# Kernel optimization log

Hardware: AMD Instinct MI355X
Metric: run time of the kernel (lower is better)

The kernel has to match this reference:

```python
import jax, jax.numpy as jnp
import numpy as np

DIM = 1024
Q_HEADS = 16
KV_HEADS = 4
DIM_HEAD = DIM // Q_HEADS  # 64
SOFTCLAMP = 50.0
EPS = 1e-8


def rotate_half(x):
    x_even = x[..., ::2]
    x_odd = x[..., 1::2]
    return jnp.stack([-x_odd, x_even], axis=-1).reshape(x.shape)


def setup_inputs() -> dict:
    key = jax.random.key(0)
    ks = jax.random.split(key, 10)
    B, S = 1, 2048
    dim_q = DIM_HEAD * Q_HEADS   # 1024
    dim_kv = DIM_HEAD * KV_HEADS  # 256
    std = 0.02
    x = jax.random.normal(ks[0], (B, S, DIM), dtype=jnp.float32)
    positions = jnp.broadcast_to(jnp.arange(S, dtype=jnp.int32)[None, :], (B, S))
    # causal mask: True = disallowed (torch semantics: allowed = ~attn_mask)
    attn_mask = jnp.triu(jnp.ones((S, S), dtype=bool), k=1)
    return {
        "x": x,
        "positions": positions,
        "attn_mask": attn_mask,
        "Wq": jax.random.normal(ks[1], (DIM, dim_q), jnp.float32) * std,
        "Wk": jax.random.normal(ks[2], (DIM, dim_kv), jnp.float32) * std,
        "Wv": jax.random.normal(ks[3], (DIM, dim_kv), jnp.float32) * std,
        "Wo": jax.random.normal(ks[4], (dim_q, DIM), jnp.float32) * std,
        "Wg": jax.random.normal(ks[5], (DIM, Q_HEADS), jnp.float32) * std,
        "Wm": jax.random.normal(ks[6], (DIM, KV_HEADS), jnp.float32) * std,
        "bm": jnp.zeros((KV_HEADS,), jnp.float32),
        "Wvr": jax.random.normal(ks[7], (DIM, dim_kv), jnp.float32) * std,
        "k_scale": jnp.ones((KV_HEADS, DIM_HEAD), jnp.float32),
    }


def reference(x, positions, attn_mask, Wq, Wk, Wv, Wo, Wg, Wm, bm, Wvr, k_scale):
    b, s, _ = x.shape
    h, qh, dh = KV_HEADS, Q_HEADS, DIM_HEAD
    g = qh // h

    q = (x @ Wq).reshape(b, s, qh, dh).transpose(0, 2, 1, 3)  # [b,qh,s,dh]
    k = (x @ Wk).reshape(b, s, h, dh).transpose(0, 2, 1, 3)   # [b,h,s,dh]
    v = (x @ Wv).reshape(b, s, h, dh).transpose(0, 2, 1, 3)

    # value-residual gating: v = lerp(v, residual_v, mix)
    residual_v = (x @ Wvr).reshape(b, s, h, dh).transpose(0, 2, 1, 3)
    mix = jax.nn.sigmoid(x @ Wm + bm).transpose(0, 2, 1)[..., None]  # [b,h,s,1]
    v = v + mix * (residual_v - v)

    # multi-head RMSNorm on k
    rms = jnp.sqrt(jnp.mean(k * k, axis=-1, keepdims=True) + EPS)
    k = k / rms * k_scale[None, :, None, :]

    # rotary embeddings (identical for all heads -> broadcast over head dim)
    inv_freq = 1.0 / (10000.0 ** (jnp.arange(0, dh, 2, dtype=jnp.float32) / dh))
    freqs = positions.astype(jnp.float32)[..., None] * inv_freq  # [b,s,dh/2]
    cos = jnp.repeat(jnp.cos(freqs), 2, axis=-1)[:, None, :, :]  # [b,1,s,dh]
    sin = jnp.repeat(jnp.sin(freqs), 2, axis=-1)[:, None, :, :]
    q = q * cos + rotate_half(q) * sin
    k = k * cos + rotate_half(k) * sin

    # grouped-query attention with softclamped scores
    scale = dh ** -0.5
    qg = q.reshape(b, h, g, s, dh)
    sim = jnp.einsum('bhgqd,bhkd->bhgqk', qg, k) * scale
    sim = jnp.tanh(sim / SOFTCLAMP) * SOFTCLAMP
    allowed = ~attn_mask  # [s,s]
    sim = jnp.where(allowed[None, None, None, :, :], sim, jnp.finfo(sim.dtype).min)
    attn = jax.nn.softmax(sim, axis=-1)
    out = jnp.einsum('bhgqk,bhkd->bhgqd', attn, v).reshape(b, qh, s, dh)

    # per-query-head sigmoid gates
    gates = jax.nn.sigmoid(x @ Wg).transpose(0, 2, 1)[..., None]  # [b,qh,s,1]
    out = out * gates

    out = out.transpose(0, 2, 1, 3).reshape(b, s, qh * dh)
    return out @ Wo
```

## Files before the change

kernel.cpp:

```cpp
#include <hip/hip_runtime.h>
#include <hip/hip_bf16.h>
#include <math.h>

typedef unsigned short u16;
typedef unsigned int u32;
typedef __attribute__((ext_vector_type(8))) __bf16 bf16x8;
typedef __attribute__((ext_vector_type(4))) float f32x4;

__device__ inline u16 f2bf(float f) {
  u32 b = __float_as_uint(f);
  b += 0x7FFFu + ((b >> 16) & 1u);
  return (u16)(b >> 16);
}
__device__ inline float bf2f(u16 b) { return __uint_as_float((u32)b << 16); }

__device__ __forceinline__ void gll16(const void* gp, void* lp) {
  __builtin_amdgcn_global_load_lds(
      (const __attribute__((address_space(1))) void*)gp,
      (__attribute__((address_space(3))) void*)lp, 16, 0, 0);
}

__global__ __launch_bounds__(256) void prep_all_k(
    const float* __restrict__ x, const int* __restrict__ positions,
    const float* __restrict__ Wq, const float* __restrict__ Wk,
    const float* __restrict__ Wv, const float* __restrict__ Wvr,
    const float* __restrict__ Wo, const float* __restrict__ Wg,
    const float* __restrict__ Wm, u16* __restrict__ xb,
    u16* __restrict__ WallT, u16* __restrict__ WoT, float* __restrict__ rtab) {
  __shared__ float tile[32][33];
  int bid = blockIdx.x, tid = threadIdx.x;
  if (bid < 1024) {
    int i = (bid * 256 + tid) * 8;
    float4 v0 = *(const float4*)&x[i];
    float4 v1 = *(const float4*)&x[i + 4];
    uint4 pk;
    pk.x = (u32)f2bf(v0.x) | ((u32)f2bf(v0.y) << 16);
    pk.y = (u32)f2bf(v0.z) | ((u32)f2bf(v0.w) << 16);
    pk.z = (u32)f2bf(v1.x) | ((u32)f2bf(v1.y) << 16);
    pk.w = (u32)f2bf(v1.z) | ((u32)f2bf(v1.w) << 16);
    *(uint4*)&xb[i] = pk;
    return;
  }
  if (bid >= 3968) {
    int idx = (bid - 3968) * 256 + tid;
    int s = idx >> 5, f = idx & 31;
    float inv = __expf(-(float)f * (9.210340371976184f / 32.f));
    float ang = (float)positions[s] * inv;
    rtab[(size_t)s * 64 + f] = cosf(ang);
    rtab[(size_t)s * 64 + 32 + f] = sinf(ang);
    return;
  }
  int b2 = bid - 1024;
  int k0 = (b2 & 31) * 32;
  int ybl = b2 >> 5;
  int tx = tid & 31, ty = tid >> 5;
  const float* src;
  int scol, sN, drow;
  u16* dst;
  if (ybl >= 60) {
    src = Wo; scol = (ybl - 60) * 32; sN = 1024; dst = WoT; drow = scol;
  } else {
    int n0 = ybl * 32;
    if (n0 >= 1792) {
#pragma unroll
      for (int j = 0; j < 4; ++j) {
        int n = n0 + ty * 4 + j, j2 = n - 1792, k = k0 + tx;
        float val = (j2 < 16) ? Wg[(size_t)k * 16 + j2]
                  : (j2 < 20) ? Wm[(size_t)k * 4 + (j2 - 16)] : 0.f;
        WallT[(size_t)n * 1024 + k] = f2bf(val);
      }
      return;
    }
    dst = WallT; drow = n0;
    if (n0 < 1024) { src = Wq; scol = n0; sN = 1024; }
    else if (n0 < 1280) { src = Wk; scol = n0 - 1024; sN = 256; }
    else if (n0 < 1536) { src = Wv; scol = n0 - 1280; sN = 256; }
    else { src = Wvr; scol = n0 - 1536; sN = 256; }
  }
#pragma unroll
  for (int j = 0; j < 4; ++j)
    tile[ty * 4 + j][tx] = src[(size_t)(k0 + ty * 4 + j) * sN + scol + tx];
  __syncthreads();
#pragma unroll
  for (int j = 0; j < 4; ++j)
    dst[(size_t)(drow + ty * 4 + j) * 1024 + k0 + tx] = f2bf(tile[tx][ty * 4 + j]);
}

template <int BM, bool BF16_OUT>
__global__ __launch_bounds__(512) void gemm_bf16_k(
    const u16* __restrict__ A, const u16* __restrict__ Bt, void* __restrict__ Cv,
    int M, int N, int K) {
  constexpr int MI = BM / 32;
  __shared__ __align__(16) u16 As[BM * 64];
  __shared__ __align__(16) u16 Bs[128 * 64];
  int tid = threadIdx.x;
  int w = tid >> 6, l = tid & 63;
  int wr = w >> 2, wc = w & 3;
  int lr = l & 15, lg = l >> 4;
  int lrow = l >> 3, lcol = (l & 7) * 8;
  int m0 = blockIdx.y * BM, n0 = blockIdx.x * 128;
  f32x4 zero = {0.f, 0.f, 0.f, 0.f};
  f32x4 acc[MI][2];
#pragma unroll
  for (int mi = 0; mi < MI; ++mi)
#pragma unroll
    for (int ni = 0; ni < 2; ++ni) acc[mi][ni] = zero;

  for (int kt = 0; kt < K; kt += 64) {
    __syncthreads();
#pragma unroll
    for (int t = 0; t < BM / 64; ++t) {
      int seg = t * 8 + w;
      gll16(&A[(size_t)(m0 + seg * 8 + lrow) * K + kt + lcol], &As[seg * 512]);
    }
#pragma unroll
    for (int t = 0; t < 2; ++t) {
      int seg = t * 8 + w;
      gll16(&Bt[(size_t)(n0 + seg * 8 + lrow) * K + kt + lcol], &Bs[seg * 512]);
    }
    __syncthreads();
#pragma unroll
    for (int kw = 0; kw < 2; ++kw) {
      bf16x8 af[MI], bfr[2];
#pragma unroll
      for (int mi = 0; mi < MI; ++mi)
        af[mi] = *(const bf16x8*)&As[(wr * (BM / 2) + mi * 16 + lr) * 64 + kw * 32 + lg * 8];
#pragma unroll
      for (int ni = 0; ni < 2; ++ni)
        bfr[ni] = *(const bf16x8*)&Bs[(wc * 32 + ni * 16 + lr) * 64 + kw * 32 + lg * 8];
#pragma unroll
      for (int mi = 0; mi < MI; ++mi)
#pragma unroll
        for (int ni = 0; ni < 2; ++ni)
          acc[mi][ni] = __builtin_amdgcn_mfma_f32_16x16x32_bf16(
              af[mi], bfr[ni], acc[mi][ni], 0, 0, 0);
    }
  }
#pragma unroll
  for (int mi = 0; mi < MI; ++mi)
#pragma unroll
    for (int ni = 0; ni < 2; ++ni)
#pragma unroll
      for (int r = 0; r < 4; ++r) {
        int row = m0 + wr * (BM / 2) + mi * 16 + lg * 4 + r;
        int col = n0 + wc * 32 + ni * 16 + lr;
        if (BF16_OUT)
          ((u16*)Cv)[(size_t)row * N + col] = f2bf(acc[mi][ni][r]);
        else
          ((float*)Cv)[(size_t)row * N + col] = acc[mi][ni][r];
      }
}

__global__ __launch_bounds__(256) void postproc_k(
    const float* __restrict__ bm, const float* __restrict__ ksc,
    const float* __restrict__ rtab, u16* __restrict__ qkvrb,
    u16* __restrict__ kb, u16* __restrict__ vb, float* __restrict__ g_out) {
  int s = blockIdx.x, tid = threadIdx.x;
  int lane = tid & 63, w = tid >> 6;
  u16* row = qkvrb + (size_t)s * 1920;
  const float* tr = rtab + (size_t)s * 64;
  if (tid < 16)
    g_out[s * 16 + tid] = 1.f / (1.f + __expf(-bf2f(row[1792 + tid])));
  int h = w, d = lane;
  float c = tr[d >> 1], sn = tr[32 + (d >> 1)];
  {
    float mixv = 1.f / (1.f + __expf(-(bf2f(row[1808 + h]) + bm[h])));
    float vv = bf2f(row[1280 + h * 64 + d]);
    float rv = bf2f(row[1536 + h * 64 + d]);
    vb[((size_t)h * 2048 + s) * 64 + d] = f2bf(vv + mixv * (rv - vv));
  }
  {
    float kv = bf2f(row[1024 + h * 64 + d]);
    float ss = kv * kv;
#pragma unroll
    for (int off = 32; off > 0; off >>= 1) ss += __shfl_xor(ss, off);
    float rms = sqrtf(ss * (1.f / 64.f) + 1e-8f);
    float kn = kv / rms * ksc[h * 64 + d];
    float partner = __shfl_xor(kn, 1);
    kb[((size_t)h * 2048 + s) * 64 + d] =
        f2bf((d & 1) ? fmaf(kn, c, partner * sn) : fmaf(kn, c, -partner * sn));
  }
#pragma unroll
  for (int r = 0; r < 4; ++r) {
    int e = r * 256 + tid;
    int dq = e & 63;
    float cq = tr[dq >> 1], sq = tr[32 + (dq >> 1)];
    float qv = bf2f(row[e]);
    float partner = __shfl_xor(qv, 1);
    float qr = (e & 1) ? fmaf(qv, cq, partner * sq) : fmaf(qv, cq, -partner * sq);
    row[e] = f2bf(qr * 0.125f);
  }
}

#define TPAD 66
__global__ __launch_bounds__(256) void vtrans_k(const u16* __restrict__ vb,
                                               u16* __restrict__ vtb) {
  __shared__ u16 tile[64 * TPAD];
  int h = blockIdx.y, s0 = blockIdx.x * 64;
  int t = threadIdx.x;
  {
    int r = t >> 2, cb = (t & 3) * 16;
    const u16* src = vb + ((size_t)h * 2048 + s0 + r) * 64 + cb;
    *(uint4*)&tile[r * TPAD + cb] = *(const uint4*)src;
    *(uint4*)&tile[r * TPAD + cb + 8] = *(const uint4*)(src + 8);
  }
  __syncthreads();
  int d = t >> 2, sb = (t & 3) * 16;
  u16 vals[16];
#pragma unroll
  for (int j = 0; j < 16; ++j) vals[j] = tile[(sb + j) * TPAD + d];
  uint4 a, b;
  a.x = (u32)vals[0] | ((u32)vals[1] << 16);
  a.y = (u32)vals[2] | ((u32)vals[3] << 16);
  a.z = (u32)vals[4] | ((u32)vals[5] << 16);
  a.w = (u32)vals[6] | ((u32)vals[7] << 16);
  b.x = (u32)vals[8] | ((u32)vals[9] << 16);
  b.y = (u32)vals[10] | ((u32)vals[11] << 16);
  b.z = (u32)vals[12] | ((u32)vals[13] << 16);
  b.w = (u32)vals[14] | ((u32)vals[15] << 16);
  u16* dst = vtb + ((size_t)h * 64 + d) * 2048 + s0 + sb;
  *(uint4*)dst = a;
  *(uint4*)(dst + 8) = b;
}

__global__ __launch_bounds__(512) void attn_k(
    const u16* __restrict__ qkvrb, const u16* __restrict__ kb,
    const u16* __restrict__ vtb, const float* __restrict__ g,
    u16* __restrict__ aob) {
  __shared__ __align__(16) u16 smem[40960];
  int head = blockIdx.x, hkv = head >> 2;
  int tid = threadIdx.x;
  int w = tid >> 6, l = tid & 63;
  int grp = w >> 2, wi = w & 3;
  int lr = l & 15, lg = l >> 4;
  int gtid = wi * 64 + l;
  u16* KsBase = smem + grp * 16384;
  u32* pw = (u32*)(smem + 32768) + (size_t)w * 512;
  float* mbuf = (float*)smem;
  f32x4 zero = {0.f, 0.f, 0.f, 0.f};
  const float C1 = 0.057707801635558534f;
  const float C2 = -144.26950408889634f;
  int sw = (lr & 7) << 2;
  int u0 = ((lg ^ (lr & 7)) << 3);
  int srow = l >> 3;
  int sunit = (l & 7) ^ srow;
  const u16* ksrc = kb + ((size_t)hkv * 2048 + srow) * 64 + sunit * 8;
  const u16* vsrc = vtb + ((size_t)(hkv * 64 + srow)) * 2048 + sunit * 8;
#pragma unroll 1
  for (int half = 0; half < 2; ++half) {
    int rb = half ? (int)blockIdx.y : (31 - (int)blockIdx.y);
    int row0 = rb * 64;
    const u16* qrow = qkvrb + (size_t)(row0 + wi * 16 + lr) * 1920 + head * 64;
    bf16x8 qf0 = *(const bf16x8*)&qrow[lg * 8];
    bf16x8 qf1 = *(const bf16x8*)&qrow[32 + lg * 8];
    f32x4 acc_o[4];
#pragma unroll
    for (int nd = 0; nd < 4; ++nd) acc_o[nd] = zero;
    float l_part = 0.f;
    int qglob = row0 + wi * 16 + lr;
    int c = grp;
    if (c <= rb) {
#pragma unroll
      for (int t = 0; t < 2; ++t) {
        int seg = wi * 2 + t;
        gll16(ksrc + (size_t)(c * 64 + seg * 8) * 64, KsBase + seg * 512);
        gll16(vsrc + (size_t)(seg * 8) * 2048 + c * 64,
              KsBase + 4096 + seg * 512);
      }
    }
    __syncthreads();
    int nmax = (rb >> 1) + 1;
#pragma unroll 1
    for (int i = 0; i < nmax; ++i, c += 2) {
      bool valid = (c <= rb);
      if (c + 2 <= rb) {
        u16* Ksn = KsBase + ((i & 1) ^ 1) * 8192;
        int nc = c + 2;
#pragma unroll
        for (int t = 0; t < 2; ++t) {
          int seg = wi * 2 + t;
          gll16(ksrc + (size_t)(nc * 64 + seg * 8) * 64, Ksn + seg * 512);
          gll16(vsrc + (size_t)(seg * 8) * 2048 + nc * 64,
                Ksn + 4096 + seg * 512);
        }
      }
      if (valid) {
        u16* Ks = KsBase + (i & 1) * 8192;
        u16* Vt = Ks + 4096;
        int kbase = c * 64;
        __builtin_amdgcn_s_setprio(1);
        f32x4 sa[4];
#pragma unroll
        for (int ni = 0; ni < 4; ++ni) {
          const u16* kp = &Ks[(ni * 16 + lr) * 64];
          bf16x8 a0 = *(const bf16x8*)&kp[u0];
          bf16x8 a1 = *(const bf16x8*)&kp[u0 ^ 32];
          f32x4 t = __builtin_amdgcn_mfma_f32_16x16x32_bf16(a0, qf0, zero, 0, 0, 0);
          sa[ni] = __builtin_amdgcn_mfma_f32_16x16x32_bf16(a1, qf1, t, 0, 0, 0);
        }
        bool diag = (c == rb);
#pragma unroll
        for (int ni = 0; ni < 4; ++ni) {
          float pv[4];
#pragma unroll
          for (int r = 0; r < 4; ++r) {
            float sv = sa[ni][r];
            float e = __builtin_amdgcn_exp2f(sv * C1);
            float p = __builtin_amdgcn_exp2f(C2 * __builtin_amdgcn_rcpf(e + 1.f));
            if (diag && (kbase + ni * 16 + lg * 4 + r) > qglob) p = 0.f;
            pv[r] = p;
            l_part += p;
          }
          u32 w0, w1;
          asm("v_cvt_pk_bf16_f32 %0, %1, %2" : "=v"(w0) : "v"(pv[0]), "v"(pv[1]));
          asm("v_cvt_pk_bf16_f32 %0, %1, %2" : "=v"(w1) : "v"(pv[2]), "v"(pv[3]));
          uint2 pr;
          pr.x = w0;
          pr.y = w1;
          *(uint2*)&pw[lr * 32 + ((ni * 8 + lg * 2) ^ sw)] = pr;
        }
        bf16x8 pfa = *(const bf16x8*)&pw[lr * 32 + ((lg * 4) ^ sw)];
        bf16x8 pfb = *(const bf16x8*)&pw[lr * 32 + ((16 + lg * 4) ^ sw)];
#pragma unroll
        for (int nd = 0; nd < 4; ++nd) {
          const u16* vp = &Vt[(nd * 16 + lr) * 64];
          bf16x8 v0 = *(const bf16x8*)&vp[u0];
          bf16x8 v1 = *(const bf16x8*)&vp[u0 ^ 32];
          acc_o[nd] = __builtin_amdgcn_mfma_f32_16x16x32_bf16(pfa, v0, acc_o[nd], 0, 0, 0);
          acc_o[nd] = __builtin_amdgcn_mfma_f32_16x16x32_bf16(pfb, v1, acc_o[nd], 0, 0, 0);
        }
        __builtin_amdgcn_s_setprio(0);
      }
      __syncthreads();
    }
    l_part += __shfl_xor(l_part, 16);
    l_part += __shfl_xor(l_part, 32);
    if (grp == 1) {
      float* mb = mbuf + (size_t)gtid * 17;
#pragma unroll
      for (int nd = 0; nd < 4; ++nd)
#pragma unroll
        for (int r = 0; r < 4; ++r) mb[nd * 4 + r] = acc_o[nd][r];
      mb[16] = l_part;
    }
    __syncthreads();
    if (grp == 0) {
      const float* mb = mbuf + (size_t)gtid * 17;
      float lt = l_part + mb[16];
#pragma unroll
      for (int r = 0; r < 4; ++r) {
        int row = row0 + wi * 16 + lg * 4 + r;
        float lv = __shfl(lt, lg * 4 + r);
        float sc = g[row * 16 + head] * __builtin_amdgcn_rcpf(lv);
#pragma unroll
        for (int nd = 0; nd < 4; ++nd)
          aob[(size_t)row * 1024 + head * 64 + nd * 16 + lr] =
              f2bf((acc_o[nd][r] + mb[nd * 4 + r]) * sc);
      }
    }
    __syncthreads();
  }
}

extern "C" void kernel_launch(void* const* d_in, const int* in_sizes, int n_in,
                              void* d_out, int out_size, void* d_ws,
                              size_t ws_size, hipStream_t stream) {
  const float* x = (const float*)d_in[0];
  const int* positions = (const int*)d_in[1];
  const float* Wq = (const float*)d_in[3];
  const float* Wk = (const float*)d_in[4];
  const float* Wv = (const float*)d_in[5];
  const float* Wo = (const float*)d_in[6];
  const float* Wg = (const float*)d_in[7];
  const float* Wm = (const float*)d_in[8];
  const float* bm = (const float*)d_in[9];
  const float* Wvr = (const float*)d_in[10];
  const float* ksc = (const float*)d_in[11];
  float* out = (float*)d_out;

  u16* xb = (u16*)d_ws;
  u16* WallT = xb + (size_t)2048 * 1024;
  u16* WoT = WallT + (size_t)1920 * 1024;
  u16* qkvrb = WoT + (size_t)1024 * 1024;
  u16* kbuf = qkvrb + (size_t)2048 * 1920;
  u16* vbuf = kbuf + (size_t)4 * 2048 * 64;
  u16* vtb = vbuf + (size_t)4 * 2048 * 64;
  float* gbuf = (float*)(vtb + (size_t)4 * 2048 * 64);
  float* rtab = gbuf + (size_t)2048 * 16;
  u16* aob = xb;

  prep_all_k<<<4224, 256, 0, stream>>>(x, positions, Wq, Wk, Wv, Wvr, Wo, Wg,
                                       Wm, xb, WallT, WoT, rtab);
  gemm_bf16_k<128, true><<<dim3(15, 16), 512, 0, stream>>>(xb, WallT, qkvrb,
                                                           2048, 1920, 1024);
  postproc_k<<<2048, 256, 0, stream>>>(bm, ksc, rtab, qkvrb, kbuf, vbuf, gbuf);
  vtrans_k<<<dim3(32, 4), 256, 0, stream>>>(vbuf, vtb);
  attn_k<<<dim3(16, 16), 512, 0, stream>>>(qkvrb, kbuf, vtb, gbuf, aob);
  gemm_bf16_k<64, false><<<dim3(8, 32), 512, 0, stream>>>(aob, WoT, out, 2048,
                                                          1024, 1024);
}
```

Before: 92.25 us.

## Process both paired query row-blocks in one pass sharing K/V tiles

After: 93.39 us. Within noise of the previous version (+1.2%).

```diff
diff --git a/kernel.cpp b/kernel.cpp
--- a/kernel.cpp
+++ b/kernel.cpp
@@ -223,12 +223,15 @@
   *(uint4*)(dst + 8) = b;
 }
 
-__global__ __launch_bounds__(512) void attn_k(
+__global__ __launch_bounds__(512, 2) void attn_k(
     const u16* __restrict__ qkvrb, const u16* __restrict__ kb,
     const u16* __restrict__ vtb, const float* __restrict__ g,
     u16* __restrict__ aob) {
   __shared__ __align__(16) u16 smem[40960];
   int head = blockIdx.x, hkv = head >> 2;
+  int by = blockIdx.y;
+  int rbH = 31 - by, rbL = by;
+  int row0H = rbH * 64, row0L = rbL * 64;
   int tid = threadIdx.x;
   int w = tid >> 6, l = tid & 63;
   int grp = w >> 2, wi = w & 3;
@@ -246,59 +249,61 @@
   int sunit = (l & 7) ^ srow;
   const u16* ksrc = kb + ((size_t)hkv * 2048 + srow) * 64 + sunit * 8;
   const u16* vsrc = vtb + ((size_t)(hkv * 64 + srow)) * 2048 + sunit * 8;
+  const u16* qrowH = qkvrb + (size_t)(row0H + wi * 16 + lr) * 1920 + head * 64;
+  const u16* qrowL = qkvrb + (size_t)(row0L + wi * 16 + lr) * 1920 + head * 64;
+  bf16x8 qfH0 = *(const bf16x8*)&qrowH[lg * 8];
+  bf16x8 qfH1 = *(const bf16x8*)&qrowH[32 + lg * 8];
+  bf16x8 qfL0 = *(const bf16x8*)&qrowL[lg * 8];
+  bf16x8 qfL1 = *(const bf16x8*)&qrowL[32 + lg * 8];
+  f32x4 accH[4], accL[4];
+#pragma unroll
+  for (int nd = 0; nd < 4; ++nd) {
+    accH[nd] = zero;
+    accL[nd] = zero;
+  }
+  float lH = 0.f, lL = 0.f;
+  int qglobH = row0H + wi * 16 + lr;
+  int qglobL = row0L + wi * 16 + lr;
+  int c = grp;
+  {
+#pragma unroll
+    for (int t = 0; t < 2; ++t) {
+      int seg = wi * 2 + t;
+      gll16(ksrc + (size_t)(c * 64 + seg * 8) * 64, KsBase + seg * 512);
+      gll16(vsrc + (size_t)(seg * 8) * 2048 + c * 64, KsBase + 4096 + seg * 512);
+    }
+  }
+  __syncthreads();
+  int nmax = (rbH >> 1) + 1;
 #pragma unroll 1
-  for (int half = 0; half < 2; ++half) {
-    int rb = half ? (int)blockIdx.y : (31 - (int)blockIdx.y);
-    int row0 = rb * 64;
-    const u16* qrow = qkvrb + (size_t)(row0 + wi * 16 + lr) * 1920 + head * 64;
-    bf16x8 qf0 = *(const bf16x8*)&qrow[lg * 8];
-    bf16x8 qf1 = *(const bf16x8*)&qrow[32 + lg * 8];
-    f32x4 acc_o[4];
-#pragma unroll
-    for (int nd = 0; nd < 4; ++nd) acc_o[nd] = zero;
-    float l_part = 0.f;
-    int qglob = row0 + wi * 16 + lr;
-    int c = grp;
-    if (c <= rb) {
+  for (int i = 0; i < nmax; ++i, c += 2) {
+    bool valid = (c <= rbH);
+    if (c + 2 <= rbH) {
+      u16* Ksn = KsBase + ((i & 1) ^ 1) * 8192;
+      int nc = c + 2;
 #pragma unroll
       for (int t = 0; t < 2; ++t) {
         int seg = wi * 2 + t;
-        gll16(ksrc + (size_t)(c * 64 + seg * 8) * 64, KsBase + seg * 512);
-        gll16(vsrc + (size_t)(seg * 8) * 2048 + c * 64,
-              KsBase + 4096 + seg * 512);
-      }
-    }
-    __syncthreads();
-    int nmax = (rb >> 1) + 1;
-#pragma unroll 1
-    for (int i = 0; i < nmax; ++i, c += 2) {
-      bool valid = (c <= rb);
-      if (c + 2 <= rb) {
-        u16* Ksn = KsBase + ((i & 1) ^ 1) * 8192;
-        int nc = c + 2;
-#pragma unroll
-        for (int t = 0; t < 2; ++t) {
-          int seg = wi * 2 + t;
-          gll16(ksrc + (size_t)(nc * 64 + seg * 8) * 64, Ksn + seg * 512);
-          gll16(vsrc + (size_t)(seg * 8) * 2048 + nc * 64,
-                Ksn + 4096 + seg * 512);
-        }
-      }
-      if (valid) {
-        u16* Ks = KsBase + (i & 1) * 8192;
-        u16* Vt = Ks + 4096;
-        int kbase = c * 64;
-        __builtin_amdgcn_s_setprio(1);
+        gll16(ksrc + (size_t)(nc * 64 + seg * 8) * 64, Ksn + seg * 512);
+        gll16(vsrc + (size_t)(seg * 8) * 2048 + nc * 64, Ksn + 4096 + seg * 512);
+      }
+    }
+    if (valid) {
+      u16* Ks = KsBase + (i & 1) * 8192;
+      u16* Vt = Ks + 4096;
+      int kbase = c * 64;
+      __builtin_amdgcn_s_setprio(1);
+      {
         f32x4 sa[4];
 #pragma unroll
         for (int ni = 0; ni < 4; ++ni) {
           const u16* kp = &Ks[(ni * 16 + lr) * 64];
           bf16x8 a0 = *(const bf16x8*)&kp[u0];
           bf16x8 a1 = *(const bf16x8*)&kp[u0 ^ 32];
-          f32x4 t = __builtin_amdgcn_mfma_f32_16x16x32_bf16(a0, qf0, zero, 0, 0, 0);
-          sa[ni] = __builtin_amdgcn_mfma_f32_16x16x32_bf16(a1, qf1, t, 0, 0, 0);
-        }
-        bool diag = (c == rb);
+          f32x4 t = __builtin_amdgcn_mfma_f32_16x16x32_bf16(a0, qfH0, zero, 0, 0, 0);
+          sa[ni] = __builtin_amdgcn_mfma_f32_16x16x32_bf16(a1, qfH1, t, 0, 0, 0);
+        }
+        bool diag = (c == rbH);
 #pragma unroll
         for (int ni = 0; ni < 4; ++ni) {
           float pv[4];
@@ -307,9 +312,9 @@
             float sv = sa[ni][r];
             float e = __builtin_amdgcn_exp2f(sv * C1);
             float p = __builtin_amdgcn_exp2f(C2 * __builtin_amdgcn_rcpf(e + 1.f));
-            if (diag && (kbase + ni * 16 + lg * 4 + r) > qglob) p = 0.f;
+            if (diag && (kbase + ni * 16 + lg * 4 + r) > qglobH) p = 0.f;
             pv[r] = p;
-            l_part += p;
+            lH += p;
           }
           u32 w0, w1;
           asm("v_cvt_pk_bf16_f32 %0, %1, %2" : "=v"(w0) : "v"(pv[0]), "v"(pv[1]));
@@ -326,39 +331,93 @@
           const u16* vp = &Vt[(nd * 16 + lr) * 64];
           bf16x8 v0 = *(const bf16x8*)&vp[u0];
           bf16x8 v1 = *(const bf16x8*)&vp[u0 ^ 32];
-          acc_o[nd] = __builtin_amdgcn_mfma_f32_16x16x32_bf16(pfa, v0, acc_o[nd], 0, 0, 0);
-          acc_o[nd] = __builtin_amdgcn_mfma_f32_16x16x32_bf16(pfb, v1, acc_o[nd], 0, 0, 0);
-        }
-        __builtin_amdgcn_s_setprio(0);
-      }
-      __syncthreads();
-    }
-    l_part += __shfl_xor(l_part, 16);
-    l_part += __shfl_xor(l_part, 32);
-    if (grp == 1) {
-      float* mb = mbuf + (size_t)gtid * 17;
-#pragma unroll
-      for (int nd = 0; nd < 4; ++nd)
-#pragma unroll
-        for (int r = 0; r < 4; ++r) mb[nd * 4 + r] = acc_o[nd][r];
-      mb[16] = l_part;
+          accH[nd] = __builtin_amdgcn_mfma_f32_16x16x32_bf16(pfa, v0, accH[nd], 0, 0, 0);
+          accH[nd] = __builtin_amdgcn_mfma_f32_16x16x32_bf16(pfb, v1, accH[nd], 0, 0, 0);
+        }
+      }
+      if (c <= rbL) {
+        f32x4 sa[4];
+#pragma unroll
+        for (int ni = 0; ni < 4; ++ni) {
+          const u16* kp = &Ks[(ni * 16 + lr) * 64];
+          bf16x8 a0 = *(const bf16x8*)&kp[u0];
+          bf16x8 a1 = *(const bf16x8*)&kp[u0 ^ 32];
+          f32x4 t = __builtin_amdgcn_mfma_f32_16x16x32_bf16(a0, qfL0, zero, 0, 0, 0);
+          sa[ni] = __builtin_amdgcn_mfma_f32_16x16x32_bf16(a1, qfL1, t, 0, 0, 0);
+        }
+        bool diag = (c == rbL);
+#pragma unroll
+        for (int ni = 0; ni < 4; ++ni) {
+          float pv[4];
+#pragma unroll
+          for (int r = 0; r < 4; ++r) {
+            float sv = sa[ni][r];
+            float e = __builtin_amdgcn_exp2f(sv * C1);
+            float p = __builtin_amdgcn_exp2f(C2 * __builtin_amdgcn_rcpf(e + 1.f));
+            if (diag && (kbase + ni * 16 + lg * 4 + r) > qglobL) p = 0.f;
+            pv[r] = p;
+            lL += p;
+          }
+          u32 w0, w1;
+          asm("v_cvt_pk_bf16_f32 %0, %1, %2" : "=v"(w0) : "v"(pv[0]), "v"(pv[1]));
+          asm("v_cvt_pk_bf16_f32 %0, %1, %2" : "=v"(w1) : "v"(pv[2]), "v"(pv[3]));
+          uint2 pr;
+          pr.x = w0;
+          pr.y = w1;
+          *(uint2*)&pw[lr * 32 + ((ni * 8 + lg * 2) ^ sw)] = pr;
+        }
+        bf16x8 pfa = *(const bf16x8*)&pw[lr * 32 + ((lg * 4) ^ sw)];
+        bf16x8 pfb = *(const bf16x8*)&pw[lr * 32 + ((16 + lg * 4) ^ sw)];
+#pragma unroll
+        for (int nd = 0; nd < 4; ++nd) {
+          const u16* vp = &Vt[(nd * 16 + lr) * 64];
+          bf16x8 v0 = *(const bf16x8*)&vp[u0];
+          bf16x8 v1 = *(const bf16x8*)&vp[u0 ^ 32];
+          accL[nd] = __builtin_amdgcn_mfma_f32_16x16x32_bf16(pfa, v0, accL[nd], 0, 0, 0);
+          accL[nd] = __builtin_amdgcn_mfma_f32_16x16x32_bf16(pfb, v1, accL[nd], 0, 0, 0);
+        }
+      }
+      __builtin_amdgcn_s_setprio(0);
     }
     __syncthreads();
-    if (grp == 0) {
-      const float* mb = mbuf + (size_t)gtid * 17;
-      float lt = l_part + mb[16];
+  }
+  lH += __shfl_xor(lH, 16);
+  lH += __shfl_xor(lH, 32);
+  lL += __shfl_xor(lL, 16);
+  lL += __shfl_xor(lL, 32);
+  if (grp == 1) {
+    float* mb = mbuf + (size_t)gtid * 34;
+#pragma unroll
+    for (int nd = 0; nd < 4; ++nd)
 #pragma unroll
       for (int r = 0; r < 4; ++r) {
-        int row = row0 + wi * 16 + lg * 4 + r;
-        float lv = __shfl(lt, lg * 4 + r);
-        float sc = g[row * 16 + head] * __builtin_amdgcn_rcpf(lv);
-#pragma unroll
-        for (int nd = 0; nd < 4; ++nd)
-          aob[(size_t)row * 1024 + head * 64 + nd * 16 + lr] =
-              f2bf((acc_o[nd][r] + mb[nd * 4 + r]) * sc);
-      }
-    }
-    __syncthreads();
+        mb[nd * 4 + r] = accH[nd][r];
+        mb[16 + nd * 4 + r] = accL[nd][r];
+      }
+    mb[32] = lH;
+    mb[33] = lL;
+  }
+  __syncthreads();
+  if (grp == 0) {
+    const float* mb = mbuf + (size_t)gtid * 34;
+    float ltH = lH + mb[32];
+    float ltL = lL + mb[33];
+#pragma unroll
+    for (int r = 0; r < 4; ++r) {
+      int rowH = row0H + wi * 16 + lg * 4 + r;
+      int rowL = row0L + wi * 16 + lg * 4 + r;
+      float lvH = __shfl(ltH, lg * 4 + r);
+      float lvL = __shfl(ltL, lg * 4 + r);
+      float scH = g[rowH * 16 + head] * __builtin_amdgcn_rcpf(lvH);
+      float scL = g[rowL * 16 + head] * __builtin_amdgcn_rcpf(lvL);
+#pragma unroll
+      for (int nd = 0; nd < 4; ++nd) {
+        aob[(size_t)rowH * 1024 + head * 64 + nd * 16 + lr] =
+            f2bf((accH[nd][r] + mb[nd * 4 + r]) * scH);
+        aob[(size_t)rowL * 1024 + head * 64 + nd * 16 + lr] =
+            f2bf((accL[nd][r] + mb[16 + nd * 4 + r]) * scL);
+      }
+    }
   }
 }
 
```

## Double-buffer LDS tiles in bf16 GEMM to overlap loads with MFMA

Applied to the files above, without the earlier changes.

New measurement: 88.06 us. -4.5%, faster.

```diff
diff --git a/kernel.cpp b/kernel.cpp
--- a/kernel.cpp
+++ b/kernel.cpp
@@ -91,8 +91,8 @@
     const u16* __restrict__ A, const u16* __restrict__ Bt, void* __restrict__ Cv,
     int M, int N, int K) {
   constexpr int MI = BM / 32;
-  __shared__ __align__(16) u16 As[BM * 64];
-  __shared__ __align__(16) u16 Bs[128 * 64];
+  __shared__ __align__(16) u16 As[2][BM * 64];
+  __shared__ __align__(16) u16 Bs[2][128 * 64];
   int tid = threadIdx.x;
   int w = tid >> 6, l = tid & 63;
   int wr = w >> 2, wc = w & 3;
@@ -106,28 +106,37 @@
 #pragma unroll
     for (int ni = 0; ni < 2; ++ni) acc[mi][ni] = zero;
 
-  for (int kt = 0; kt < K; kt += 64) {
-    __syncthreads();
-#pragma unroll
-    for (int t = 0; t < BM / 64; ++t) {
-      int seg = t * 8 + w;
-      gll16(&A[(size_t)(m0 + seg * 8 + lrow) * K + kt + lcol], &As[seg * 512]);
-    }
-#pragma unroll
-    for (int t = 0; t < 2; ++t) {
-      int seg = t * 8 + w;
-      gll16(&Bt[(size_t)(n0 + seg * 8 + lrow) * K + kt + lcol], &Bs[seg * 512]);
-    }
-    __syncthreads();
+  auto gstage = [&](int buf, int kt) {
+#pragma unroll
+    for (int ts = 0; ts < BM / 64; ++ts) {
+      int seg = ts * 8 + w;
+      gll16(&A[(size_t)(m0 + seg * 8 + lrow) * K + kt + lcol],
+            &As[buf][seg * 512]);
+    }
+#pragma unroll
+    for (int ts = 0; ts < 2; ++ts) {
+      int seg = ts * 8 + w;
+      gll16(&Bt[(size_t)(n0 + seg * 8 + lrow) * K + kt + lcol],
+            &Bs[buf][seg * 512]);
+    }
+  };
+
+  gstage(0, 0);
+  __syncthreads();
+  int nt = K >> 6;
+#pragma unroll 1
+  for (int t = 0; t < nt; ++t) {
+    int cur = t & 1;
+    if (t + 1 < nt) gstage(cur ^ 1, (t + 1) * 64);
 #pragma unroll
     for (int kw = 0; kw < 2; ++kw) {
       bf16x8 af[MI], bfr[2];
 #pragma unroll
       for (int mi = 0; mi < MI; ++mi)
-        af[mi] = *(const bf16x8*)&As[(wr * (BM / 2) + mi * 16 + lr) * 64 + kw * 32 + lg * 8];
+        af[mi] = *(const bf16x8*)&As[cur][(wr * (BM / 2) + mi * 16 + lr) * 64 + kw * 32 + lg * 8];
 #pragma unroll
       for (int ni = 0; ni < 2; ++ni)
-        bfr[ni] = *(const bf16x8*)&Bs[(wc * 32 + ni * 16 + lr) * 64 + kw * 32 + lg * 8];
+        bfr[ni] = *(const bf16x8*)&Bs[cur][(wc * 32 + ni * 16 + lr) * 64 + kw * 32 + lg * 8];
 #pragma unroll
       for (int mi = 0; mi < MI; ++mi)
 #pragma unroll
@@ -135,6 +144,7 @@
           acc[mi][ni] = __builtin_amdgcn_mfma_f32_16x16x32_bf16(
               af[mi], bfr[ni], acc[mi][ni], 0, 0, 0);
     }
+    __syncthreads();
   }
 #pragma unroll
   for (int mi = 0; mi < MI; ++mi)
```
